# Performance work log

Measured on AMD Instinct MI355X. Metric: run time of the kernel, lower is better.

Reference implementation:

```python
import jax, jax.numpy as jnp
import numpy as np

DIM = 1024
HEADS = 16
HEAD_DIM = DIM // HEADS


def _rope(x, cos, sin):
    # x: [B, H, L, Dh]; cos/sin: [L, Dh//2]
    x1 = x[..., ::2]
    x2 = x[..., 1::2]
    xr1 = x1 * cos - x2 * sin
    xr2 = x1 * sin + x2 * cos
    # interleave back: stack on last dim then flatten -> [..., Dh]
    return jnp.stack([xr1, xr2], axis=-1).reshape(x.shape)


def setup_inputs() -> dict:
    key = jax.random.key(0)
    k1, k2, k3 = jax.random.split(key, 3)
    B, L = 4, 2048
    x = jax.random.normal(k1, (B, L, DIM), dtype=jnp.float32)
    # weights stored [in, out]; scaled like kaiming-ish init
    w_qkv = jax.random.normal(k2, (DIM, 3 * DIM), dtype=jnp.float32) / np.sqrt(DIM)
    w_proj = jax.random.normal(k3, (DIM, DIM), dtype=jnp.float32) / np.sqrt(DIM)
    return {"x": x, "w_qkv": w_qkv, "w_proj": w_proj}


def reference(x, w_qkv, w_proj):
    B, L, D = x.shape
    H, Dh = HEADS, HEAD_DIM

    qkv = x @ w_qkv                      # [B, L, 3D]
    q, k, v = jnp.split(qkv, 3, axis=-1)

    def reshape(t):
        return t.reshape(B, L, H, Dh).transpose(0, 2, 1, 3)  # [B, H, L, Dh]

    q, k, v = reshape(q), reshape(k), reshape(v)

    # RoPE tables
    theta = 10000.0
    inv_freq = 1.0 / theta ** (jnp.arange(0, Dh, 2, dtype=jnp.float32) / Dh)
    t = jnp.arange(L, dtype=jnp.float32)
    freqs = jnp.einsum('l,d->ld', t, inv_freq)   # [L, Dh//2]
    cos, sin = jnp.cos(freqs), jnp.sin(freqs)

    q = _rope(q, cos, sin)
    k = _rope(k, cos, sin)

    scale = 1.0 / np.sqrt(Dh).astype(np.float32)
    attn = jnp.einsum('bhqd,bhkd->bhqk', q, k) * scale   # [B, H, L, L]
    attn = jax.nn.softmax(attn, axis=-1)
    out = jnp.einsum('bhqk,bhkd->bhqd', attn, v)          # [B, H, L, Dh]
    out = out.transpose(0, 2, 1, 3).reshape(B, L, D)
    return out @ w_proj
```

## Files before the change

### kernel.cpp

```cpp
#include <hip/hip_runtime.h>

#define L_SEQ   2048
#define D_MODEL 1024
#define N_QKV   3072

typedef __attribute__((ext_vector_type(8)))  short short8;
typedef __attribute__((ext_vector_type(4)))  float f32x4;
typedef __attribute__((ext_vector_type(16))) float f32x16;

__device__ __forceinline__ unsigned short f2bf(float f){
    unsigned int u = __float_as_uint(f);
    u += 0x7fffu + ((u >> 16) & 1u);
    return (unsigned short)(u >> 16);
}

__device__ __forceinline__ void gload16(const void* g, void* l){
    __builtin_amdgcn_global_load_lds(
        (const __attribute__((address_space(1))) unsigned int*)g,
        (__attribute__((address_space(3))) unsigned int*)l, 16, 0, 0);
}

__device__ __forceinline__ unsigned int cvtpk_bf16(float lo, float hi){
    unsigned int r;
    asm volatile("v_cvt_pk_bf16_f32 %0, %1, %2" : "=v"(r) : "v"(lo), "v"(hi));
    return r;
}

__global__ void rope_table_kernel(float* __restrict__ cost, float* __restrict__ sint){
    int idx = blockIdx.x * blockDim.x + threadIdx.x;
    if (idx >= L_SEQ * 32) return;
    int l = idx >> 5;
    int i = idx & 31;
    double e = (double)(2 * i) / 64.0;
    float invf = (float)pow(10000.0, -e);
    float f = (float)l * invf;
    cost[idx] = cosf(f);
    sint[idx] = sinf(f);
}

__global__ __launch_bounds__(256) void cvt_bf16_kernel(
    const float* __restrict__ in, unsigned short* __restrict__ out)
{
    int i = (blockIdx.x * 256 + threadIdx.x) * 4;
    float4 v = *(const float4*)(in + i);
    ushort4 o;
    o.x = f2bf(v.x); o.y = f2bf(v.y); o.z = f2bf(v.z); o.w = f2bf(v.w);
    *(ushort4*)(out + i) = o;
}

__global__ __launch_bounds__(256) void transpose_bf16_kernel(
    const float* __restrict__ W, unsigned short* __restrict__ WT, int K, int N)
{
    __shared__ float T[64][65];
    const int k0 = blockIdx.y * 64, n0 = blockIdx.x * 64;
    const int r  = threadIdx.x >> 4;
    const int c4 = (threadIdx.x & 15) * 4;
    #pragma unroll
    for (int i = 0; i < 4; ++i){
        int row = r + i * 16;
        float4 v = *(const float4*)&W[(size_t)(k0 + row) * N + n0 + c4];
        T[row][c4 + 0] = v.x; T[row][c4 + 1] = v.y;
        T[row][c4 + 2] = v.z; T[row][c4 + 3] = v.w;
    }
    __syncthreads();
    #pragma unroll
    for (int i = 0; i < 4; ++i){
        int nl = r + i * 16;
        ushort4 o;
        o.x = f2bf(T[c4 + 0][nl]); o.y = f2bf(T[c4 + 1][nl]);
        o.z = f2bf(T[c4 + 2][nl]); o.w = f2bf(T[c4 + 3][nl]);
        *(ushort4*)&WT[(size_t)(n0 + nl) * K + k0 + c4] = o;
    }
}

__global__ __launch_bounds__(512, 4) void qkv_mfma_kernel(
    const unsigned short* __restrict__ A, const unsigned short* __restrict__ BT,
    const float* __restrict__ cost, const float* __restrict__ sint,
    unsigned short* __restrict__ qb, unsigned short* __restrict__ kb,
    unsigned short* __restrict__ vtb)
{
    __shared__ __align__(16) unsigned char smem[34816];
    unsigned short* Al = (unsigned short*)smem;
    unsigned short* Bl = Al + 8192;
    unsigned short* T  = (unsigned short*)smem;

    const int tid  = threadIdx.x;
    const int lane = tid & 63;
    const int w    = tid >> 6;
    const int wm   = w & 1, wn = w >> 1;
    const int l15  = lane & 15, l4 = lane >> 4;
    const int m0   = blockIdx.y * 128;
    const int n0   = blockIdx.x * 128;

    const int srow = tid >> 3;
    const int scol = ((tid & 7) * 8) ^ ((srow & 7) * 8);
    const int ksw  = (l15 & 7) * 8;

    f32x4 acc[4][2];
    #pragma unroll
    for (int i = 0; i < 4; ++i)
        #pragma unroll
        for (int j = 0; j < 2; ++j)
            acc[i][j] = (f32x4){0.f, 0.f, 0.f, 0.f};

    for (int k0 = 0; k0 < 1024; k0 += 64){
        #pragma unroll
        for (int c = 0; c < 2; ++c){
            gload16(&A [(size_t)(m0 + c * 64 + srow) * 1024 + k0 + scol],
                    &Al[c * 4096 + w * 512]);
            gload16(&BT[(size_t)(n0 + c * 64 + srow) * 1024 + k0 + scol],
                    &Bl[c * 4096 + w * 512]);
        }
        __syncthreads();
        #pragma unroll
        for (int kc = 0; kc < 2; ++kc){
            short8 a[4], b[2];
            #pragma unroll
            for (int mi = 0; mi < 4; ++mi)
                a[mi] = *(const short8*)&Al[(wm * 64 + mi * 16 + l15) * 64 + ((kc * 32 + l4 * 8) ^ ksw)];
            #pragma unroll
            for (int ni = 0; ni < 2; ++ni)
                b[ni] = *(const short8*)&Bl[(wn * 32 + ni * 16 + l15) * 64 + ((kc * 32 + l4 * 8) ^ ksw)];
            #pragma unroll
            for (int mi = 0; mi < 4; ++mi)
                #pragma unroll
                for (int ni = 0; ni < 2; ++ni)
                    acc[mi][ni] = __builtin_amdgcn_mfma_f32_16x16x32_bf16(a[mi], b[ni], acc[mi][ni], 0, 0, 0);
        }
        __syncthreads();
    }

    const int which = n0 >> 10;
    #pragma unroll
    for (int ni = 0; ni < 2; ++ni){
        const int c  = wn * 32 + ni * 16 + l15;
        const int d  = (n0 + c) & 63;
        const int fi = d >> 1;
        const float sgn = (d & 1) ? 1.0f : -1.0f;
        #pragma unroll
        for (int mi = 0; mi < 4; ++mi){
            const int row0 = wm * 64 + mi * 16 + l4 * 4;
            if (which == 2){
                ushort4 pk;
                pk.x = f2bf(acc[mi][ni][0]); pk.y = f2bf(acc[mi][ni][1]);
                pk.z = f2bf(acc[mi][ni][2]); pk.w = f2bf(acc[mi][ni][3]);
                *(ushort4*)&T[c * 136 + row0] = pk;
            } else {
                #pragma unroll
                for (int r = 0; r < 4; ++r){
                    int row = row0 + r;
                    int gl  = (m0 + row) & 2047;
                    float val = acc[mi][ni][r];
                    float cs = cost[gl * 32 + fi];
                    float sn = sint[gl * 32 + fi];
                    float partner = __shfl_xor(val, 1);
                    float outv = val * cs + sgn * partner * sn;
                    if (which == 0) outv *= 0.125f;
                    T[row * 136 + c] = f2bf(outv);
                }
            }
        }
    }
    __syncthreads();

    const int bidx = m0 >> 11;
    if (which == 2){
        #pragma unroll
        for (int it = 0; it < 4; ++it){
            int chunk = it * 512 + tid;
            int crow  = chunk >> 4;
            int lch   = chunk & 15;
            short8 v = *(const short8*)&T[crow * 136 + lch * 8];
            int colg = n0 + crow;
            int hh   = (colg & 1023) >> 6;
            int d    = colg & 63;
            int l0   = (m0 & 2047) + lch * 8;
            *(short8*)&vtb[(((size_t)(bidx * 16 + hh)) * 64 + d) * 2048 + l0] = v;
        }
    } else {
        unsigned short* dstb = (which == 0) ? qb : kb;
        #pragma unroll
        for (int it = 0; it < 4; ++it){
            int chunk = it * 512 + tid;
            int row   = chunk >> 4;
            int ch    = chunk & 15;
            short8 v = *(const short8*)&T[row * 136 + ch * 8];
            int gl   = (m0 & 2047) + row;
            int colg = n0 + ch * 8;
            int hh   = (colg & 1023) >> 6;
            int d0   = colg & 63;
            *(short8*)&dstb[(((size_t)(bidx * 16 + hh)) * 2048 + gl) * 64 + d0] = v;
        }
    }
}

__global__ __launch_bounds__(256, 3) void proj_mfma_kernel(
    const unsigned short* __restrict__ A, const unsigned short* __restrict__ BT,
    float* __restrict__ C)
{
    __shared__ __align__(16) unsigned short Al[128 * 64];
    __shared__ __align__(16) unsigned short Bl[128 * 64];

    const int tid  = threadIdx.x;
    const int lane = tid & 63;
    const int w    = tid >> 6;
    const int wm   = w & 1, wn = w >> 1;
    const int l15  = lane & 15, l4 = lane >> 4;
    const int m0   = blockIdx.y * 128;
    const int n0   = blockIdx.x * 128;

    const int srow = tid >> 3;
    const int scol = ((tid & 7) * 8) ^ ((srow & 7) * 8);
    const int ksw  = (l15 & 7) * 8;

    f32x4 acc[4][4];
    #pragma unroll
    for (int i = 0; i < 4; ++i)
        #pragma unroll
        for (int j = 0; j < 4; ++j)
            acc[i][j] = (f32x4){0.f, 0.f, 0.f, 0.f};

    for (int k0 = 0; k0 < 1024; k0 += 64){
        #pragma unroll
        for (int c = 0; c < 4; ++c){
            gload16(&A [(size_t)(m0 + c * 32 + srow) * 1024 + k0 + scol],
                    &Al[c * 2048 + w * 512]);
            gload16(&BT[(size_t)(n0 + c * 32 + srow) * 1024 + k0 + scol],
                    &Bl[c * 2048 + w * 512]);
        }
        __syncthreads();
        #pragma unroll
        for (int kc = 0; kc < 2; ++kc){
            short8 a[4], b[4];
            #pragma unroll
            for (int mi = 0; mi < 4; ++mi)
                a[mi] = *(const short8*)&Al[(wm * 64 + mi * 16 + l15) * 64 + ((kc * 32 + l4 * 8) ^ ksw)];
            #pragma unroll
            for (int ni = 0; ni < 4; ++ni)
                b[ni] = *(const short8*)&Bl[(wn * 64 + ni * 16 + l15) * 64 + ((kc * 32 + l4 * 8) ^ ksw)];
            #pragma unroll
            for (int mi = 0; mi < 4; ++mi)
                #pragma unroll
                for (int ni = 0; ni < 4; ++ni)
                    acc[mi][ni] = __builtin_amdgcn_mfma_f32_16x16x32_bf16(a[mi], b[ni], acc[mi][ni], 0, 0, 0);
        }
        __syncthreads();
    }

    #pragma unroll
    for (int mi = 0; mi < 4; ++mi)
        #pragma unroll
        for (int r = 0; r < 4; ++r){
            int row = m0 + wm * 64 + mi * 16 + l4 * 4 + r;
            #pragma unroll
            for (int ni = 0; ni < 4; ++ni){
                int colc = n0 + wn * 64 + ni * 16 + l15;
                C[(size_t)row * 1024 + colc] = acc[mi][ni][r];
            }
        }
}

__global__ __launch_bounds__(512, 4) void attn_mfma32_kernel(
    const unsigned short* __restrict__ qb,
    const unsigned short* __restrict__ kb,
    const unsigned short* __restrict__ vtb,
    unsigned short* __restrict__ ctx)
{
    __shared__ __align__(16) unsigned char lds[49152];

    const int tid  = threadIdx.x;
    const int lane = tid & 63;
    const int w    = tid >> 6;
    const int l31  = lane & 31;
    const int hi   = lane >> 5;
    const int blk = blockIdx.x;
    const int swz = ((blk & 7) << 6) | (blk >> 3);
    const int bh  = swz >> 3;
    const int qt  = swz & 7;
    const int b   = bh >> 4, h = bh & 15;

    const unsigned short* Kg  = kb  + (size_t)bh * 2048 * 64;
    const unsigned short* VTg = vtb + (size_t)bh * 64 * 2048;
    const int q0 = qt * 256 + w * 32;
    const unsigned short* Qg = qb + ((size_t)bh * 2048 + q0) * 64;

    short8 qf[4];
    #pragma unroll
    for (int kbd = 0; kbd < 4; ++kbd)
        qf[kbd] = *(const short8*)(Qg + l31 * 64 + hi * 8 + kbd * 16);

    f32x16 o0, o1;
    f32x4  lsv = (f32x4){0.f, 0.f, 0.f, 0.f};
    #pragma unroll
    for (int r = 0; r < 16; ++r){ o0[r] = 0.f; o1[r] = 0.f; }

    const unsigned short* ksrc = Kg + ((size_t)((w >> 2) * 32 + l31)) * 64 + hi * 8 + (w & 3) * 16;
    const unsigned short* vsrc = VTg + ((size_t)((w >> 2) * 32 + l31)) * 2048 + hi * 8 + (w & 3) * 16;

    auto STAGE = [&](int t, int buf){
        unsigned char* base = lds + buf * 16384 + w * 1024;
        gload16(ksrc + (size_t)t * 4096, base);
        gload16(vsrc + (size_t)t * 64, base + 8192);
    };

    STAGE(0, 0);
    STAGE(1, 1);

    int bufc = 0;
    for (int t = 0; t < 32; ++t){
        if (t < 31){
            asm volatile("s_waitcnt vmcnt(2)" ::: "memory");
        } else {
            asm volatile("s_waitcnt vmcnt(0)" ::: "memory");
        }
        __builtin_amdgcn_s_barrier();
        if (t < 30) STAGE(t + 2, (bufc == 0) ? 2 : bufc - 1);

        unsigned char* Kl = lds + bufc * 16384;
        unsigned char* Vl = Kl + 8192;

        f32x16 s0, s1;
        #pragma unroll
        for (int r = 0; r < 16; ++r){ s0[r] = -16.0f; s1[r] = -16.0f; }
        __builtin_amdgcn_s_setprio(1);
        #pragma unroll
        for (int kbd = 0; kbd < 4; ++kbd){
            short8 kfA = *(const short8*)(Kl + (0 * 4 + kbd) * 1024 + lane * 16);
            short8 kfB = *(const short8*)(Kl + (1 * 4 + kbd) * 1024 + lane * 16);
            s0 = __builtin_amdgcn_mfma_f32_32x32x16_bf16(kfA, qf[kbd], s0, 0, 0, 0);
            s1 = __builtin_amdgcn_mfma_f32_32x32x16_bf16(kfB, qf[kbd], s1, 0, 0, 0);
        }
        __builtin_amdgcn_s_setprio(0);

        #pragma unroll
        for (int r = 0; r < 16; ++r){
            float p0 = __expf(s0[r]);
            float p1 = __expf(s1[r]);
            s0[r] = p0; s1[r] = p1;
            lsv[r & 3] += p0 + p1;
        }

        short8 pa[4];
        #pragma unroll
        for (int half = 0; half < 2; ++half){
            unsigned int w01 = cvtpk_bf16(s0[half*8+0], s0[half*8+1]);
            unsigned int w23 = cvtpk_bf16(s0[half*8+2], s0[half*8+3]);
            unsigned int w45 = cvtpk_bf16(s0[half*8+4], s0[half*8+5]);
            unsigned int w67 = cvtpk_bf16(s0[half*8+6], s0[half*8+7]);
            asm volatile("v_permlane32_swap_b32 %0, %1" : "+v"(w01), "+v"(w45));
            asm volatile("v_permlane32_swap_b32 %0, %1" : "+v"(w23), "+v"(w67));
            short8 pp;
            pp[0] = (short)(w01 & 0xffffu); pp[1] = (short)(w01 >> 16);
            pp[2] = (short)(w23 & 0xffffu); pp[3] = (short)(w23 >> 16);
            pp[4] = (short)(w45 & 0xffffu); pp[5] = (short)(w45 >> 16);
            pp[6] = (short)(w67 & 0xffffu); pp[7] = (short)(w67 >> 16);
            pa[half] = pp;
        }
        #pragma unroll
        for (int half = 0; half < 2; ++half){
            unsigned int w01 = cvtpk_bf16(s1[half*8+0], s1[half*8+1]);
            unsigned int w23 = cvtpk_bf16(s1[half*8+2], s1[half*8+3]);
            unsigned int w45 = cvtpk_bf16(s1[half*8+4], s1[half*8+5]);
            unsigned int w67 = cvtpk_bf16(s1[half*8+6], s1[half*8+7]);
            asm volatile("v_permlane32_swap_b32 %0, %1" : "+v"(w01), "+v"(w45));
            asm volatile("v_permlane32_swap_b32 %0, %1" : "+v"(w23), "+v"(w67));
            short8 pp;
            pp[0] = (short)(w01 & 0xffffu); pp[1] = (short)(w01 >> 16);
            pp[2] = (short)(w23 & 0xffffu); pp[3] = (short)(w23 >> 16);
            pp[4] = (short)(w45 & 0xffffu); pp[5] = (short)(w45 >> 16);
            pp[6] = (short)(w67 & 0xffffu); pp[7] = (short)(w67 >> 16);
            pa[2 + half] = pp;
        }

        #pragma unroll
        for (int kbv = 0; kbv < 4; ++kbv){
            short8 vf0 = *(const short8*)(Vl + (0 * 4 + kbv) * 1024 + lane * 16);
            short8 vf1 = *(const short8*)(Vl + (1 * 4 + kbv) * 1024 + lane * 16);
            __builtin_amdgcn_s_setprio(1);
            o0 = __builtin_amdgcn_mfma_f32_32x32x16_bf16(vf0, pa[kbv], o0, 0, 0, 0);
            o1 = __builtin_amdgcn_mfma_f32_32x32x16_bf16(vf1, pa[kbv], o1, 0, 0, 0);
            __builtin_amdgcn_s_setprio(0);
        }

        bufc = (bufc == 2) ? 0 : bufc + 1;
    }

    float ls = lsv[0] + lsv[1] + lsv[2] + lsv[3];
    ls += __shfl_xor(ls, 32);
    float inv = 1.0f / ls;

    size_t crow = (size_t)b * 2048 + q0 + l31;
    unsigned short* cp = ctx + crow * 1024 + h * 64;
    #pragma unroll
    for (int r = 0; r < 16; ++r){
        int d = (r & 3) + 8 * (r >> 2) + 4 * hi;
        cp[d]      = f2bf(o0[r] * inv);
        cp[d + 32] = f2bf(o1[r] * inv);
    }
}

extern "C" void kernel_launch(void* const* d_in, const int* in_sizes, int n_in,
                              void* d_out, int out_size, void* d_ws, size_t ws_size,
                              hipStream_t stream) {
    const float* x      = (const float*)d_in[0];
    const float* w_qkv  = (const float*)d_in[1];
    const float* w_proj = (const float*)d_in[2];
    float* out = (float*)d_out;

    char* ws = (char*)d_ws;
    float*          cost   = (float*)(ws);
    float*          sint   = (float*)(ws + 262144);
    unsigned short* xbf    = (unsigned short*)(ws + 524288);
    unsigned short* qb     = (unsigned short*)(ws + 17301504);
    unsigned short* kb     = (unsigned short*)(ws + 34078720);
    unsigned short* vtb    = (unsigned short*)(ws + 50855936);
    unsigned short* wqkvT  = (unsigned short*)(ws + 67633152);
    unsigned short* wprojT = (unsigned short*)(ws + 73924608);
    unsigned short* ctxbf  = xbf;

    rope_table_kernel<<<256, 256, 0, stream>>>(cost, sint);

    cvt_bf16_kernel<<<8192, 256, 0, stream>>>(x, xbf);

    dim3 gt1(48, 16);
    transpose_bf16_kernel<<<gt1, 256, 0, stream>>>(w_qkv, wqkvT, 1024, 3072);
    dim3 gt2(16, 16);
    transpose_bf16_kernel<<<gt2, 256, 0, stream>>>(w_proj, wprojT, 1024, 1024);

    dim3 g1(24, 64);
    qkv_mfma_kernel<<<g1, 512, 0, stream>>>(xbf, wqkvT, cost, sint, qb, kb, vtb);

    attn_mfma32_kernel<<<512, 512, 0, stream>>>(qb, kb, vtb, ctxbf);

    dim3 g3(8, 64);
    proj_mfma_kernel<<<g3, 256, 0, stream>>>(ctxbf, wprojT, out);
}
```

Measured before the change: 186.6 us.

## Double-buffer 128-key tiles in attention instead of triple-buffered 64-key tiles

The attention loop now stages 128 keys per iteration into two 32KB LDS buffers, replacing a three-deep ring of 64-key tiles. This halves the number of barriers and iterations, and each barrier now covers two unrolled softmax/PV sub-steps. The trade-off is shallower prefetch: the loop waits with vmcnt(0) instead of keeping two tiles in flight. LDS per block also grows to 64KB, which may limit how many blocks can reside on each CU.

```diff
diff --git a/kernel.cpp b/kernel.cpp
--- a/kernel.cpp
+++ b/kernel.cpp
@@ -266,7 +266,7 @@
     const unsigned short* __restrict__ vtb,
     unsigned short* __restrict__ ctx)
 {
-    __shared__ __align__(16) unsigned char lds[49152];
+    __shared__ __align__(16) unsigned char lds[65536];
 
     const int tid  = threadIdx.x;
     const int lane = tid & 63;
@@ -294,95 +294,95 @@
     #pragma unroll
     for (int r = 0; r < 16; ++r){ o0[r] = 0.f; o1[r] = 0.f; }
 
-    const unsigned short* ksrc = Kg + ((size_t)((w >> 2) * 32 + l31)) * 64 + hi * 8 + (w & 3) * 16;
-    const unsigned short* vsrc = VTg + ((size_t)((w >> 2) * 32 + l31)) * 2048 + hi * 8 + (w & 3) * 16;
+    const int r0i = 2 * w, r1i = 2 * w + 1;
+    const unsigned short* ksrc0 = Kg + ((size_t)((r0i >> 2) * 32 + l31)) * 64 + hi * 8 + (r0i & 3) * 16;
+    const unsigned short* ksrc1 = Kg + ((size_t)((r1i >> 2) * 32 + l31)) * 64 + hi * 8 + (r1i & 3) * 16;
+    const unsigned short* vsrc0 = VTg + ((size_t)(((r0i >> 2) & 1) * 32 + l31)) * 2048 + (r0i >> 3) * 64 + (r0i & 3) * 16 + hi * 8;
+    const unsigned short* vsrc1 = VTg + ((size_t)(((r1i >> 2) & 1) * 32 + l31)) * 2048 + (r1i >> 3) * 64 + (r1i & 3) * 16 + hi * 8;
 
     auto STAGE = [&](int t, int buf){
-        unsigned char* base = lds + buf * 16384 + w * 1024;
-        gload16(ksrc + (size_t)t * 4096, base);
-        gload16(vsrc + (size_t)t * 64, base + 8192);
+        unsigned char* base = lds + buf * 32768;
+        gload16(ksrc0 + (size_t)t * 8192, base + r0i * 1024);
+        gload16(ksrc1 + (size_t)t * 8192, base + r1i * 1024);
+        gload16(vsrc0 + (size_t)t * 128, base + 16384 + r0i * 1024);
+        gload16(vsrc1 + (size_t)t * 128, base + 16384 + r1i * 1024);
     };
 
     STAGE(0, 0);
-    STAGE(1, 1);
-
-    int bufc = 0;
-    for (int t = 0; t < 32; ++t){
-        if (t < 31){
-            asm volatile("s_waitcnt vmcnt(2)" ::: "memory");
-        } else {
-            asm volatile("s_waitcnt vmcnt(0)" ::: "memory");
-        }
+
+    for (int t = 0; t < 16; ++t){
+        asm volatile("s_waitcnt vmcnt(0)" ::: "memory");
         __builtin_amdgcn_s_barrier();
-        if (t < 30) STAGE(t + 2, (bufc == 0) ? 2 : bufc - 1);
-
-        unsigned char* Kl = lds + bufc * 16384;
-        unsigned char* Vl = Kl + 8192;
-
-        f32x16 s0, s1;
-        #pragma unroll
-        for (int r = 0; r < 16; ++r){ s0[r] = -16.0f; s1[r] = -16.0f; }
-        __builtin_amdgcn_s_setprio(1);
-        #pragma unroll
-        for (int kbd = 0; kbd < 4; ++kbd){
-            short8 kfA = *(const short8*)(Kl + (0 * 4 + kbd) * 1024 + lane * 16);
-            short8 kfB = *(const short8*)(Kl + (1 * 4 + kbd) * 1024 + lane * 16);
-            s0 = __builtin_amdgcn_mfma_f32_32x32x16_bf16(kfA, qf[kbd], s0, 0, 0, 0);
-            s1 = __builtin_amdgcn_mfma_f32_32x32x16_bf16(kfB, qf[kbd], s1, 0, 0, 0);
-        }
-        __builtin_amdgcn_s_setprio(0);
-
-        #pragma unroll
-        for (int r = 0; r < 16; ++r){
-            float p0 = __expf(s0[r]);
-            float p1 = __expf(s1[r]);
-            s0[r] = p0; s1[r] = p1;
-            lsv[r & 3] += p0 + p1;
-        }
-
-        short8 pa[4];
-        #pragma unroll
-        for (int half = 0; half < 2; ++half){
-            unsigned int w01 = cvtpk_bf16(s0[half*8+0], s0[half*8+1]);
-            unsigned int w23 = cvtpk_bf16(s0[half*8+2], s0[half*8+3]);
-            unsigned int w45 = cvtpk_bf16(s0[half*8+4], s0[half*8+5]);
-            unsigned int w67 = cvtpk_bf16(s0[half*8+6], s0[half*8+7]);
-            asm volatile("v_permlane32_swap_b32 %0, %1" : "+v"(w01), "+v"(w45));
-            asm volatile("v_permlane32_swap_b32 %0, %1" : "+v"(w23), "+v"(w67));
-            short8 pp;
-            pp[0] = (short)(w01 & 0xffffu); pp[1] = (short)(w01 >> 16);
-            pp[2] = (short)(w23 & 0xffffu); pp[3] = (short)(w23 >> 16);
-            pp[4] = (short)(w45 & 0xffffu); pp[5] = (short)(w45 >> 16);
-            pp[6] = (short)(w67 & 0xffffu); pp[7] = (short)(w67 >> 16);
-            pa[half] = pp;
-        }
-        #pragma unroll
-        for (int half = 0; half < 2; ++half){
-            unsigned int w01 = cvtpk_bf16(s1[half*8+0], s1[half*8+1]);
-            unsigned int w23 = cvtpk_bf16(s1[half*8+2], s1[half*8+3]);
-            unsigned int w45 = cvtpk_bf16(s1[half*8+4], s1[half*8+5]);
-            unsigned int w67 = cvtpk_bf16(s1[half*8+6], s1[half*8+7]);
-            asm volatile("v_permlane32_swap_b32 %0, %1" : "+v"(w01), "+v"(w45));
-            asm volatile("v_permlane32_swap_b32 %0, %1" : "+v"(w23), "+v"(w67));
-            short8 pp;
-            pp[0] = (short)(w01 & 0xffffu); pp[1] = (short)(w01 >> 16);
-            pp[2] = (short)(w23 & 0xffffu); pp[3] = (short)(w23 >> 16);
-            pp[4] = (short)(w45 & 0xffffu); pp[5] = (short)(w45 >> 16);
-            pp[6] = (short)(w67 & 0xffffu); pp[7] = (short)(w67 >> 16);
-            pa[2 + half] = pp;
-        }
-
-        #pragma unroll
-        for (int kbv = 0; kbv < 4; ++kbv){
-            short8 vf0 = *(const short8*)(Vl + (0 * 4 + kbv) * 1024 + lane * 16);
-            short8 vf1 = *(const short8*)(Vl + (1 * 4 + kbv) * 1024 + lane * 16);
+        if (t < 15) STAGE(t + 1, (t & 1) ^ 1);
+
+        unsigned char* Kl = lds + (t & 1) * 32768;
+        unsigned char* Vl = Kl + 16384;
+
+        #pragma unroll
+        for (int s = 0; s < 2; ++s){
+            f32x16 s0, s1;
+            #pragma unroll
+            for (int r = 0; r < 16; ++r){ s0[r] = -16.0f; s1[r] = -16.0f; }
             __builtin_amdgcn_s_setprio(1);
-            o0 = __builtin_amdgcn_mfma_f32_32x32x16_bf16(vf0, pa[kbv], o0, 0, 0, 0);
-            o1 = __builtin_amdgcn_mfma_f32_32x32x16_bf16(vf1, pa[kbv], o1, 0, 0, 0);
+            #pragma unroll
+            for (int kbd = 0; kbd < 4; ++kbd){
+                short8 kfA = *(const short8*)(Kl + (s * 8 + 0 * 4 + kbd) * 1024 + lane * 16);
+                short8 kfB = *(const short8*)(Kl + (s * 8 + 1 * 4 + kbd) * 1024 + lane * 16);
+                s0 = __builtin_amdgcn_mfma_f32_32x32x16_bf16(kfA, qf[kbd], s0, 0, 0, 0);
+                s1 = __builtin_amdgcn_mfma_f32_32x32x16_bf16(kfB, qf[kbd], s1, 0, 0, 0);
+            }
             __builtin_amdgcn_s_setprio(0);
-        }
-
-        bufc = (bufc == 2) ? 0 : bufc + 1;
+
+            #pragma unroll
+            for (int r = 0; r < 16; ++r){
+                float p0 = __expf(s0[r]);
+                float p1 = __expf(s1[r]);
+                s0[r] = p0; s1[r] = p1;
+                lsv[r & 3] += p0 + p1;
+            }
+
+            short8 pa[4];
+            #pragma unroll
+            for (int half = 0; half < 2; ++half){
+                unsigned int w01 = cvtpk_bf16(s0[half*8+0], s0[half*8+1]);
+                unsigned int w23 = cvtpk_bf16(s0[half*8+2], s0[half*8+3]);
+                unsigned int w45 = cvtpk_bf16(s0[half*8+4], s0[half*8+5]);
+                unsigned int w67 = cvtpk_bf16(s0[half*8+6], s0[half*8+7]);
+                asm volatile("v_permlane32_swap_b32 %0, %1" : "+v"(w01), "+v"(w45));
+                asm volatile("v_permlane32_swap_b32 %0, %1" : "+v"(w23), "+v"(w67));
+                short8 pp;
+                pp[0] = (short)(w01 & 0xffffu); pp[1] = (short)(w01 >> 16);
+                pp[2] = (short)(w23 & 0xffffu); pp[3] = (short)(w23 >> 16);
+                pp[4] = (short)(w45 & 0xffffu); pp[5] = (short)(w45 >> 16);
+                pp[6] = (short)(w67 & 0xffffu); pp[7] = (short)(w67 >> 16);
+                pa[half] = pp;
+            }
+            #pragma unroll
+            for (int half = 0; half < 2; ++half){
+                unsigned int w01 = cvtpk_bf16(s1[half*8+0], s1[half*8+1]);
+                unsigned int w23 = cvtpk_bf16(s1[half*8+2], s1[half*8+3]);
+                unsigned int w45 = cvtpk_bf16(s1[half*8+4], s1[half*8+5]);
+                unsigned int w67 = cvtpk_bf16(s1[half*8+6], s1[half*8+7]);
+                asm volatile("v_permlane32_swap_b32 %0, %1" : "+v"(w01), "+v"(w45));
+                asm volatile("v_permlane32_swap_b32 %0, %1" : "+v"(w23), "+v"(w67));
+                short8 pp;
+                pp[0] = (short)(w01 & 0xffffu); pp[1] = (short)(w01 >> 16);
+                pp[2] = (short)(w23 & 0xffffu); pp[3] = (short)(w23 >> 16);
+                pp[4] = (short)(w45 & 0xffffu); pp[5] = (short)(w45 >> 16);
+                pp[6] = (short)(w67 & 0xffffu); pp[7] = (short)(w67 >> 16);
+                pa[2 + half] = pp;
+            }
+
+            #pragma unroll
+            for (int kbv = 0; kbv < 4; ++kbv){
+                short8 vf0 = *(const short8*)(Vl + (s * 8 + 0 * 4 + kbv) * 1024 + lane * 16);
+                short8 vf1 = *(const short8*)(Vl + (s * 8 + 1 * 4 + kbv) * 1024 + lane * 16);
+                __builtin_amdgcn_s_setprio(1);
+                o0 = __builtin_amdgcn_mfma_f32_32x32x16_bf16(vf0, pa[kbv], o0, 0, 0, 0);
+                o1 = __builtin_amdgcn_mfma_f32_32x32x16_bf16(vf1, pa[kbv], o1, 0, 0, 0);
+                __builtin_amdgcn_s_setprio(0);
+            }
+        }
     }
 
     float ls = lsv[0] + lsv[1] + lsv[2] + lsv[3];
```

New measurement: 228.2 us. 22.3% more time.
